# Optimization experiments

Measured on AMD Instinct MI355X. Metric: run time of the kernel, lower is better.

Reference implementation:

```python
import jax, jax.numpy as jnp
import numpy as np

C = 32
SHIFTS = (1, 2, 4)
KSIZE = 4  # trans_layer: kernel KSIZE+1, stride KSIZE, pad KSIZE//2
EPS_NORM = 1e-12
EPS_BN = 1e-5


def _make_diff_kernels(c):
    # 8 fixed 3x3 difference kernels, tiled per channel for depthwise conv.
    d1 = np.array([[[-1, 0, 0], [0, 1, 0], [0, 0, 0]],
                   [[0, -1, 0], [0, 1, 0], [0, 0, 0]],
                   [[0, 0, -1], [0, 1, 0], [0, 0, 0]],
                   [[0, 0, 0], [0, 1, -1], [0, 0, 0]]], dtype=np.float32)
    d1 = d1.reshape(4, 1, 3, 3)
    d2 = d1[:, :, ::-1, ::-1].copy()
    delta = np.concatenate([d1, d2], axis=0)          # [8,1,3,3]
    return jnp.asarray(np.tile(delta, (c, 1, 1, 1)))  # [8C,1,3,3]


DIFF_KERNELS = _make_diff_kernels(C)


def conv2d(x, w, stride=1, pad=0, dilation=1, groups=1):
    return jax.lax.conv_general_dilated(
        x, w, (stride, stride), [(pad, pad), (pad, pad)],
        rhs_dilation=(dilation, dilation),
        dimension_numbers=('NCHW', 'OIHW', 'NCHW'),
        feature_group_count=groups)


def l2norm(x, axis=-1):
    n = jnp.sqrt(jnp.sum(x * x, axis=axis, keepdims=True))
    return x / jnp.maximum(n, EPS_NORM)


def setup_inputs() -> dict:
    key = jax.random.key(0)
    ks = jax.random.split(key, 8)
    S = len(SHIFTS)
    return {
        'cen': jax.random.normal(ks[0], (2, C, 256, 256), jnp.float32),
        'trans_W': jax.random.normal(ks[1], (C, C, 5, 5), jnp.float32) * 0.05,
        'trans_b': jax.random.normal(ks[2], (C,), jnp.float32) * 0.05,
        'query_W': jax.random.normal(ks[3], (C, C, 1, 1), jnp.float32) * 0.05,
        'value_W': jax.random.normal(ks[4], (S, C, C, 1, 1), jnp.float32) * 0.05,
        'key_W': jax.random.normal(ks[5], (S, C, C, 1, 1), jnp.float32) * 0.05,
        'out_W': jax.random.normal(ks[6], (C, C, 1, 1), jnp.float32) * 0.05,
        'bn_gamma': jnp.ones((C,), jnp.float32),
        'bn_beta': jnp.zeros((C,), jnp.float32),
        'bn_mean': jnp.zeros((C,), jnp.float32),
        'bn_var': jnp.ones((C,), jnp.float32),
    }


def reference(cen, trans_W, trans_b, query_W, value_W, key_W, out_W,
              bn_gamma, bn_beta, bn_mean, bn_var):
    b, _, w, h = cen.shape
    S = len(SHIFTS)
    size = (w * h) // (KSIZE * KSIZE)

    # trans_layer: kernel KSIZE+1, stride KSIZE, pad KSIZE//2
    kv_cen = conv2d(cen, trans_W, stride=KSIZE, pad=KSIZE // 2) \
        + trans_b[None, :, None, None]

    keys, values = [], []
    for i, d in enumerate(SHIFTS):
        v = conv2d(cen, value_W[i])          # [b,C,w,h]
        k = conv2d(kv_cen, key_W[i])         # [b,C,w',h']
        # depthwise dilated difference conv -> 8 outputs per channel
        v = conv2d(v, DIFF_KERNELS, pad=d, dilation=d, groups=C)  # [b,8C,w,h]
        k = conv2d(k, DIFF_KERNELS, pad=d, dilation=d, groups=C)  # [b,8C,w',h']
        keys.append(k)
        values.append(v)

    querys = conv2d(kv_cen, query_W)  # [b,C,w',h']

    keys = jnp.stack(keys, axis=2).reshape(b, C, 8 * S, size)       # [b,C,8S,size]
    values = jnp.stack(values, axis=2).reshape(b, C, 8 * S, w * h)  # [b,C,8S,wh]

    keys = jnp.swapaxes(l2norm(keys, -1), -2, -1)        # [b,C,size,8S]
    querys = l2norm(querys.reshape(b, C, 1, size), -1)   # [b,C,1,size]

    score = jnp.matmul(querys, keys)   # [b,C,1,8S]  cosine sims
    score = l2norm(score, -1)
    out = jnp.matmul(score, values).reshape(b, C, w, h)

    # out_conv: 1x1 conv -> BN (eval mode, running stats) -> ReLU
    out = conv2d(out, out_W)
    inv = jax.lax.rsqrt(bn_var + EPS_BN)
    out = (out - bn_mean[None, :, None, None]) * (bn_gamma * inv)[None, :, None, None] \
        + bn_beta[None, :, None, None]
    return jax.nn.relu(out)
```

## Files before the change

kernel.cpp:

```cpp
#include <hip/hip_runtime.h>
#include <hip/hip_bf16.h>


#define CC 32
#define HW 256
#define KVW 64
#define VTS 100

__global__ __launch_bounds__(256, 2) void k1_trans(const float* __restrict__ cen,
                                                   const float* __restrict__ tW,
                                                   const float* __restrict__ tB,
                                                   float* __restrict__ kv) {
  __shared__ alignas(16) float part[4][4][64];
  int bid = blockIdx.x;
  int b = bid >> 9, cog = (bid >> 6) & 7, y = bid & 63;
  int tid = threadIdx.x;
  int x = tid & 63;
  int w = __builtin_amdgcn_readfirstlane(tid >> 6);
  int ci0 = w * 8;
  int co0 = cog * 4;

  float acc[4] = {0.f, 0.f, 0.f, 0.f};
  const float4 z4 = {0.f, 0.f, 0.f, 0.f};

  int roff[5];
  bool rok[5];
#pragma unroll
  for (int r = 0; r < 5; r++) {
    int row = 4 * y - 2 + r;
    rok[r] = (row >= 0);
    roff[r] = (row < 0 ? 0 : row) * HW;
  }

  for (int cc4 = 0; cc4 < 8; cc4 += 4) {
    int ci = ci0 + cc4;
    const float* pc[4];
#pragma unroll
    for (int c = 0; c < 4; c++) pc[c] = cen + (size_t)(b * CC + ci + c) * 65536 + 4 * x;
    float4 A[4][5], B[4][5];
#pragma unroll
    for (int c = 0; c < 4; c++) {
#pragma unroll
      for (int r = 0; r < 5; r++) {
        A[c][r] = (x > 0) ? *(const float4*)(pc[c] + roff[r] - 4) : z4;
        B[c][r] = *(const float4*)(pc[c] + roff[r]);
      }
    }
#pragma unroll
    for (int r = 0; r < 5; r++) {
      if (!rok[r]) continue;
#pragma unroll
      for (int c = 0; c < 4; c++) {
#pragma unroll
        for (int co = 0; co < 4; co++) {
          const float* wa = tW + ((co0 + co) * CC + ci + c) * 25 + r * 5;
          acc[co] += wa[0] * A[c][r].z + wa[1] * A[c][r].w + wa[2] * B[c][r].x +
                     wa[3] * B[c][r].y + wa[4] * B[c][r].z;
        }
      }
    }
  }

#pragma unroll
  for (int co = 0; co < 4; co++) part[w][co][x] = acc[co];
  __syncthreads();
  {
    int co = tid >> 6, xx = tid & 63;
    float s = part[0][co][xx] + part[1][co][xx] + part[2][co][xx] + part[3][co][xx];
    kv[((b * CC + co0 + co) * KVW + y) * KVW + xx] = s + tB[co0 + co];
  }
}

__device__ inline float wred64(float v) {
#pragma unroll
  for (int off = 1; off < 64; off <<= 1) v += __shfl_xor(v, off);
  return v;
}

__global__ __launch_bounds__(1024) void k23_fat(const float* __restrict__ kv,
                                                const float* __restrict__ qW,
                                                const float* __restrict__ kW,
                                                float* __restrict__ srraw,
                                                const float* __restrict__ cen,
                                                const float* __restrict__ vW,
                                                __hip_bfloat16* __restrict__ v) {
  __shared__ alignas(16) float kl[4096];
  __shared__ float wredl[16][18];
  int bid = blockIdx.x;
  int tid = threadIdx.x;
  int g = bid / 7, s = bid - g * 7;

  if (s < 3) {
    int k2id = g * 3 + s;
    int bc = k2id / 3, i = k2id - bc * 3;
    int b = bc >> 5, c = bc & 31;
    int lane = tid & 63, w = tid >> 6;
    int xx = tid & 63;
    int ybase = tid >> 6;

    float qreg[4];
#pragma unroll
    for (int r = 0; r < 4; r++) {
      int px = r * 1024 + tid;
      float q = 0.f, kk = 0.f;
#pragma unroll
      for (int ci = 0; ci < CC; ci++) {
        float val = kv[(b * CC + ci) * 4096 + px];
        q += qW[c * CC + ci] * val;
        kk += kW[(i * CC + c) * CC + ci] * val;
      }
      qreg[r] = q;
      kl[px] = kk;
    }
    __syncthreads();

    float q2 = 0.f;
#pragma unroll
    for (int r = 0; r < 4; r++) q2 += qreg[r] * qreg[r];
    q2 = wred64(q2);
    if (lane == 0) wredl[w][16] = q2;

    constexpr int DYt[8] = {-1, -1, -1, 0, 1, 1, 1, 0};
    constexpr int DXt[8] = {-1, 0, 1, 1, 1, 0, -1, -1};
    const int d = 1 << i;
#pragma unroll
    for (int n = 0; n < 8; n++) {
      const int dy = DYt[n], dx = DXt[n];
      int xn = xx + dx * d;
      bool xok = (xn >= 0 && xn < KVW);
      float dacc = 0.f, macc = 0.f;
#pragma unroll
      for (int r = 0; r < 4; r++) {
        int yy = r * 16 + ybase;
        int px = yy * KVW + xx;
        float kc = kl[px];
        int yn = yy + dy * d;
        float kn = (xok && yn >= 0 && yn < KVW) ? kl[yn * KVW + xn] : 0.f;
        float df = kc - kn;
        dacc += qreg[r] * df;
        macc += df * df;
      }
      dacc = wred64(dacc);
      macc = wred64(macc);
      if (lane == 0) {
        wredl[w][n] = dacc;
        wredl[w][8 + n] = macc;
      }
    }
    __syncthreads();

    if (tid < 8) {
      float D = 0.f, M = 0.f, Q = 0.f;
      for (int w2 = 0; w2 < 16; w2++) {
        D += wredl[w2][tid];
        M += wredl[w2][8 + tid];
        Q += wredl[w2][16];
      }
      float sr = D / (fmaxf(sqrtf(M), 1e-12f) * fmaxf(sqrtf(Q), 1e-12f));
      srraw[bc * 24 + i * 8 + tid] = sr;
    }
  } else {
    int k3id = g * 4 + (s - 3);
    int vb = k3id * 4 + (tid >> 8);
    int b = vb >> 9, blk = vb & 511;
    int lane = tid & 63;
    int cg = __builtin_amdgcn_readfirstlane((tid >> 6) & 3);
    int px = blk * 128 + lane * 2;

    float2 cr[CC];
#pragma unroll
    for (int ci = 0; ci < CC; ci++)
      cr[ci] = *(const float2*)(cen + (size_t)(b * CC + ci) * 65536 + px);

#pragma unroll
    for (int i = 0; i < 3; i++) {
#pragma unroll
      for (int cc = 0; cc < 8; cc++) {
        int c = cg * 8 + cc;
        const float* wp = vW + (i * CC + c) * CC;
        float a0 = 0.f, a1 = 0.f;
#pragma unroll
        for (int ci = 0; ci < CC; ci++) {
          a0 += wp[ci] * cr[ci].x;
          a1 += wp[ci] * cr[ci].y;
        }
        __hip_bfloat16 h0 = __float2bfloat16(a0);
        __hip_bfloat16 h1 = __float2bfloat16(a1);
        unsigned int pk = (unsigned int)(*(unsigned short*)&h0) |
                          ((unsigned int)(*(unsigned short*)&h1) << 16);
        *(unsigned int*)((unsigned short*)v + (((size_t)((i * 2 + b) * CC + c)) << 16) +
                         px) = pk;
      }
    }
  }
}

__global__ __launch_bounds__(256) void k3b_combine(const __hip_bfloat16* __restrict__ v,
                                                   const float* __restrict__ srraw,
                                                   const float* __restrict__ oW,
                                                   const float* __restrict__ gamma,
                                                   const float* __restrict__ beta,
                                                   const float* __restrict__ mean,
                                                   const float* __restrict__ var,
                                                   float* __restrict__ out) {
  __shared__ alignas(16) float vt[3 * 24 * VTS];
  __shared__ alignas(16) float sl[27][32];
  __shared__ alignas(16) float owl[32][32];
  __shared__ float bns[32], bnb[32];

  int bid = blockIdx.x;
  int b = bid >> 8, tile = bid & 255;
  int ty = tile >> 4, tx = tile & 15;
  int tid = threadIdx.x;
  int ly = tid >> 4, lx = tid & 15;

  for (int f = tid; f < 768; f += 256) {
    int j = f >> 5, c = f & 31;
    sl[j][c] = srraw[(b * CC + c) * 24 + j];
  }
  for (int f = tid; f < 1024; f += 256) owl[f >> 5][f & 31] = oW[f];
  if (tid < 32) {
    float inv = rsqrtf(var[tid] + 1e-5f);
    float sc = gamma[tid] * inv;
    bns[tid] = sc;
    bnb[tid] = beta[tid] - mean[tid] * sc;
  }
  __syncthreads();
  if (tid < 32) {
    float r2 = 0.f;
#pragma unroll
    for (int j = 0; j < 24; j++) {
      float s = sl[j][tid];
      r2 += s * s;
    }
    float dn = fmaxf(sqrtf(r2), 1e-12f);
#pragma unroll
    for (int j = 0; j < 24; j++) sl[j][tid] /= dn;
#pragma unroll
    for (int i = 0; i < 3; i++) {
      float s = 0.f;
      for (int n = 0; n < 8; n++) s += sl[i * 8 + n][tid];
      sl[24 + i][tid] = s;
    }
  }

  int ldsoff[4], pxoff[4], ibase[4];
  bool okp[4];
#pragma unroll
  for (int it = 0; it < 4; it++) {
    int p = tid + it * 256;
    bool act = (p < 864);
    int pp = act ? p : 0;
    int i = pp / 288;
    int rem = pp - i * 288;
    int r = rem / 12;
    int col = (rem - r * 12) * 2;
    int gy = ty * 16 + r - 4, gx = tx * 16 + col - 4;
    okp[it] = act && gy >= 0 && gy < HW && gx >= 0 && gx < HW;
    pxoff[it] = gy * HW + gx;
    ibase[it] = (i * 2 + b) * CC;
    ldsoff[it] = (i * 24 + r) * VTS + col * 4;
  }

  constexpr int DYt[8] = {-1, -1, -1, 0, 1, 1, 1, 0};
  constexpr int DXt[8] = {-1, 0, 1, 1, 1, 0, -1, -1};

  float acc[32];
#pragma unroll
  for (int co = 0; co < 32; co++) acc[co] = 0.f;

  unsigned int pf[4][4];
  const unsigned short* vs = (const unsigned short*)v;

#pragma unroll
  for (int it = 0; it < 4; it++)
#pragma unroll
    for (int cp = 0; cp < 4; cp++)
      pf[it][cp] = okp[it]
                       ? *(const unsigned int*)(vs + (((size_t)(ibase[it] + cp)) << 16) +
                                                pxoff[it])
                       : 0u;

  for (int cg = 0; cg < 8; cg++) {
    __syncthreads();
#pragma unroll
    for (int it = 0; it < 4; it++) {
      if (it == 3 && tid >= 96) continue;
      float4 lo, hi;
      lo.x = __uint_as_float(pf[it][0] << 16);
      lo.y = __uint_as_float(pf[it][1] << 16);
      lo.z = __uint_as_float(pf[it][2] << 16);
      lo.w = __uint_as_float(pf[it][3] << 16);
      hi.x = __uint_as_float(pf[it][0] & 0xffff0000u);
      hi.y = __uint_as_float(pf[it][1] & 0xffff0000u);
      hi.z = __uint_as_float(pf[it][2] & 0xffff0000u);
      hi.w = __uint_as_float(pf[it][3] & 0xffff0000u);
      *(float4*)&vt[ldsoff[it]] = lo;
      *(float4*)&vt[ldsoff[it] + 4] = hi;
    }
    if (cg < 7) {
      int cb = (cg + 1) * 4;
#pragma unroll
      for (int it = 0; it < 4; it++)
#pragma unroll
        for (int cp = 0; cp < 4; cp++)
          pf[it][cp] = okp[it] ? *(const unsigned int*)(vs +
                                                        (((size_t)(ibase[it] + cb + cp))
                                                         << 16) +
                                                        pxoff[it])
                               : 0u;
    }
    __syncthreads();

    float4 pre = {0.f, 0.f, 0.f, 0.f};
#pragma unroll
    for (int i = 0; i < 3; i++) {
      const int d = 1 << i;
      float4 S4 = *(const float4*)&sl[24 + i][cg * 4];
      float4 ctr = *(const float4*)&vt[(i * 24 + (ly + 4)) * VTS + (lx + 4) * 4];
      pre.x += S4.x * ctr.x;
      pre.y += S4.y * ctr.y;
      pre.z += S4.z * ctr.z;
      pre.w += S4.w * ctr.w;
#pragma unroll
      for (int n = 0; n < 8; n++) {
        float4 sj = *(const float4*)&sl[i * 8 + n][cg * 4];
        float4 nb = *(const float4*)&vt[(i * 24 + (ly + 4 + DYt[n] * d)) * VTS +
                                        (lx + 4 + DXt[n] * d) * 4];
        pre.x -= sj.x * nb.x;
        pre.y -= sj.y * nb.y;
        pre.z -= sj.z * nb.z;
        pre.w -= sj.w * nb.w;
      }
    }
#pragma unroll
    for (int co = 0; co < 32; co++) {
      float4 ow = *(const float4*)&owl[co][cg * 4];
      acc[co] += ow.x * pre.x + ow.y * pre.y + ow.z * pre.z + ow.w * pre.w;
    }
  }

  int gy = ty * 16 + ly, gx = tx * 16 + lx;
#pragma unroll
  for (int co = 0; co < 32; co++) {
    float val = acc[co] * bns[co] + bnb[co];
    out[((size_t)(b * CC + co) << 16) + gy * HW + gx] = fmaxf(val, 0.f);
  }
}

extern "C" void kernel_launch(void* const* d_in, const int* in_sizes, int n_in,
                              void* d_out, int out_size, void* d_ws, size_t ws_size,
                              hipStream_t stream) {
  const float* cen = (const float*)d_in[0];
  const float* trans_W = (const float*)d_in[1];
  const float* trans_b = (const float*)d_in[2];
  const float* query_W = (const float*)d_in[3];
  const float* value_W = (const float*)d_in[4];
  const float* key_W = (const float*)d_in[5];
  const float* out_W = (const float*)d_in[6];
  const float* bn_gamma = (const float*)d_in[7];
  const float* bn_beta = (const float*)d_in[8];
  const float* bn_mean = (const float*)d_in[9];
  const float* bn_var = (const float*)d_in[10];
  float* out = (float*)d_out;

  float* kv = (float*)d_out;
  float* srraw = (float*)d_ws;
  __hip_bfloat16* v = (__hip_bfloat16*)((char*)d_ws + 532480);

  k1_trans<<<1024, 256, 0, stream>>>(cen, trans_W, trans_b, kv);
  k23_fat<<<448, 1024, 0, stream>>>(kv, query_W, key_W, srraw, cen, value_W, v);
  k3b_combine<<<512, 256, 0, stream>>>(v, srraw, out_W, bn_gamma, bn_beta, bn_mean,
                                       bn_var, out);
}
```

Measured before the change: 161.1 us.

## Store value tensor channel-last bf16 and read stencil neighbors directly from global

The value projection now writes bf16 values in a pixel-major, channel-contiguous layout (32 channels per pixel) using 16-byte vector stores. The combine kernel drops the LDS halo tile, its double-buffered prefetch and its per-channel-group syncs. Each thread instead loads each neighbor's 32 channels as four uint4 reads straight from global/L2. It also folds the negation into the normalized scores, reads out_W from global instead of LDS, and swizzles the block order. This trades LDS staging and barriers for more redundant global/cache traffic across the 27 stencil taps.

```diff
diff --git a/kernel.cpp b/kernel.cpp
--- a/kernel.cpp
+++ b/kernel.cpp
@@ -5,7 +5,6 @@
 #define CC 32
 #define HW 256
 #define KVW 64
-#define VTS 100
 
 __global__ __launch_bounds__(256, 2) void k1_trans(const float* __restrict__ cen,
                                                    const float* __restrict__ tW,
@@ -172,25 +171,38 @@
     for (int ci = 0; ci < CC; ci++)
       cr[ci] = *(const float2*)(cen + (size_t)(b * CC + ci) * 65536 + px);
 
+    unsigned short* vo = (unsigned short*)v;
 #pragma unroll
     for (int i = 0; i < 3; i++) {
-#pragma unroll
-      for (int cc = 0; cc < 8; cc++) {
-        int c = cg * 8 + cc;
-        const float* wp = vW + (i * CC + c) * CC;
-        float a0 = 0.f, a1 = 0.f;
+      unsigned int d0[4], d1[4];
+#pragma unroll
+      for (int cp = 0; cp < 4; cp++) {
+        int c0 = cg * 8 + cp * 2;
+        const float* wpA = vW + (i * CC + c0) * CC;
+        const float* wpB = wpA + CC;
+        float a0A = 0.f, a1A = 0.f, a0B = 0.f, a1B = 0.f;
 #pragma unroll
         for (int ci = 0; ci < CC; ci++) {
-          a0 += wp[ci] * cr[ci].x;
-          a1 += wp[ci] * cr[ci].y;
+          a0A += wpA[ci] * cr[ci].x;
+          a1A += wpA[ci] * cr[ci].y;
+          a0B += wpB[ci] * cr[ci].x;
+          a1B += wpB[ci] * cr[ci].y;
         }
-        __hip_bfloat16 h0 = __float2bfloat16(a0);
-        __hip_bfloat16 h1 = __float2bfloat16(a1);
-        unsigned int pk = (unsigned int)(*(unsigned short*)&h0) |
-                          ((unsigned int)(*(unsigned short*)&h1) << 16);
-        *(unsigned int*)((unsigned short*)v + (((size_t)((i * 2 + b) * CC + c)) << 16) +
-                         px) = pk;
-      }
+        __hip_bfloat16 hA0 = __float2bfloat16(a0A);
+        __hip_bfloat16 hB0 = __float2bfloat16(a0B);
+        __hip_bfloat16 hA1 = __float2bfloat16(a1A);
+        __hip_bfloat16 hB1 = __float2bfloat16(a1B);
+        d0[cp] = (unsigned int)(*(unsigned short*)&hA0) |
+                 ((unsigned int)(*(unsigned short*)&hB0) << 16);
+        d1[cp] = (unsigned int)(*(unsigned short*)&hA1) |
+                 ((unsigned int)(*(unsigned short*)&hB1) << 16);
+      }
+      size_t base = ((size_t)((i * 2 + b) * 65536 + px)) * 32 + cg * 8;
+      uint4 q0, q1;
+      q0.x = d0[0]; q0.y = d0[1]; q0.z = d0[2]; q0.w = d0[3];
+      q1.x = d1[0]; q1.y = d1[1]; q1.z = d1[2]; q1.w = d1[3];
+      *(uint4*)(vo + base) = q0;
+      *(uint4*)(vo + base + 32) = q1;
     }
   }
 }
@@ -203,22 +215,21 @@
                                                    const float* __restrict__ mean,
                                                    const float* __restrict__ var,
                                                    float* __restrict__ out) {
-  __shared__ alignas(16) float vt[3 * 24 * VTS];
   __shared__ alignas(16) float sl[27][32];
-  __shared__ alignas(16) float owl[32][32];
   __shared__ float bns[32], bnb[32];
 
-  int bid = blockIdx.x;
+  int bid0 = blockIdx.x;
+  int bid = (bid0 & 7) * 64 + (bid0 >> 3);
   int b = bid >> 8, tile = bid & 255;
   int ty = tile >> 4, tx = tile & 15;
   int tid = threadIdx.x;
   int ly = tid >> 4, lx = tid & 15;
+  int y = ty * 16 + ly, x = tx * 16 + lx;
 
   for (int f = tid; f < 768; f += 256) {
     int j = f >> 5, c = f & 31;
     sl[j][c] = srraw[(b * CC + c) * 24 + j];
   }
-  for (int f = tid; f < 1024; f += 256) owl[f >> 5][f & 31] = oW[f];
   if (tid < 32) {
     float inv = rsqrtf(var[tid] + 1e-5f);
     float sc = gamma[tid] * inv;
@@ -235,116 +246,72 @@
     }
     float dn = fmaxf(sqrtf(r2), 1e-12f);
 #pragma unroll
-    for (int j = 0; j < 24; j++) sl[j][tid] /= dn;
-#pragma unroll
     for (int i = 0; i < 3; i++) {
-      float s = 0.f;
-      for (int n = 0; n < 8; n++) s += sl[i * 8 + n][tid];
-      sl[24 + i][tid] = s;
-    }
-  }
-
-  int ldsoff[4], pxoff[4], ibase[4];
-  bool okp[4];
-#pragma unroll
-  for (int it = 0; it < 4; it++) {
-    int p = tid + it * 256;
-    bool act = (p < 864);
-    int pp = act ? p : 0;
-    int i = pp / 288;
-    int rem = pp - i * 288;
-    int r = rem / 12;
-    int col = (rem - r * 12) * 2;
-    int gy = ty * 16 + r - 4, gx = tx * 16 + col - 4;
-    okp[it] = act && gy >= 0 && gy < HW && gx >= 0 && gx < HW;
-    pxoff[it] = gy * HW + gx;
-    ibase[it] = (i * 2 + b) * CC;
-    ldsoff[it] = (i * 24 + r) * VTS + col * 4;
-  }
+      float ssum = 0.f;
+#pragma unroll
+      for (int n = 0; n < 8; n++) {
+        float sn = sl[i * 8 + n][tid] / dn;
+        sl[i * 8 + n][tid] = -sn;
+        ssum += sn;
+      }
+      sl[24 + i][tid] = ssum;
+    }
+  }
+  __syncthreads();
 
   constexpr int DYt[8] = {-1, -1, -1, 0, 1, 1, 1, 0};
   constexpr int DXt[8] = {-1, 0, 1, 1, 1, 0, -1, -1};
 
-  float acc[32];
-#pragma unroll
-  for (int co = 0; co < 32; co++) acc[co] = 0.f;
-
-  unsigned int pf[4][4];
   const unsigned short* vs = (const unsigned short*)v;
-
-#pragma unroll
-  for (int it = 0; it < 4; it++)
-#pragma unroll
-    for (int cp = 0; cp < 4; cp++)
-      pf[it][cp] = okp[it]
-                       ? *(const unsigned int*)(vs + (((size_t)(ibase[it] + cp)) << 16) +
-                                                pxoff[it])
-                       : 0u;
-
-  for (int cg = 0; cg < 8; cg++) {
-    __syncthreads();
-#pragma unroll
-    for (int it = 0; it < 4; it++) {
-      if (it == 3 && tid >= 96) continue;
-      float4 lo, hi;
-      lo.x = __uint_as_float(pf[it][0] << 16);
-      lo.y = __uint_as_float(pf[it][1] << 16);
-      lo.z = __uint_as_float(pf[it][2] << 16);
-      lo.w = __uint_as_float(pf[it][3] << 16);
-      hi.x = __uint_as_float(pf[it][0] & 0xffff0000u);
-      hi.y = __uint_as_float(pf[it][1] & 0xffff0000u);
-      hi.z = __uint_as_float(pf[it][2] & 0xffff0000u);
-      hi.w = __uint_as_float(pf[it][3] & 0xffff0000u);
-      *(float4*)&vt[ldsoff[it]] = lo;
-      *(float4*)&vt[ldsoff[it] + 4] = hi;
-    }
-    if (cg < 7) {
-      int cb = (cg + 1) * 4;
-#pragma unroll
-      for (int it = 0; it < 4; it++)
-#pragma unroll
-        for (int cp = 0; cp < 4; cp++)
-          pf[it][cp] = okp[it] ? *(const unsigned int*)(vs +
-                                                        (((size_t)(ibase[it] + cb + cp))
-                                                         << 16) +
-                                                        pxoff[it])
-                               : 0u;
-    }
-    __syncthreads();
-
-    float4 pre = {0.f, 0.f, 0.f, 0.f};
-#pragma unroll
-    for (int i = 0; i < 3; i++) {
-      const int d = 1 << i;
-      float4 S4 = *(const float4*)&sl[24 + i][cg * 4];
-      float4 ctr = *(const float4*)&vt[(i * 24 + (ly + 4)) * VTS + (lx + 4) * 4];
-      pre.x += S4.x * ctr.x;
-      pre.y += S4.y * ctr.y;
-      pre.z += S4.z * ctr.z;
-      pre.w += S4.w * ctr.w;
-#pragma unroll
-      for (int n = 0; n < 8; n++) {
-        float4 sj = *(const float4*)&sl[i * 8 + n][cg * 4];
-        float4 nb = *(const float4*)&vt[(i * 24 + (ly + 4 + DYt[n] * d)) * VTS +
-                                        (lx + 4 + DXt[n] * d) * 4];
-        pre.x -= sj.x * nb.x;
-        pre.y -= sj.y * nb.y;
-        pre.z -= sj.z * nb.z;
-        pre.w -= sj.w * nb.w;
-      }
-    }
-#pragma unroll
-    for (int co = 0; co < 32; co++) {
-      float4 ow = *(const float4*)&owl[co][cg * 4];
-      acc[co] += ow.x * pre.x + ow.y * pre.y + ow.z * pre.z + ow.w * pre.w;
-    }
-  }
-
-  int gy = ty * 16 + ly, gx = tx * 16 + lx;
-#pragma unroll
-  for (int co = 0; co < 32; co++) {
-    float val = acc[co] * bns[co] + bnb[co];
-    out[((size_t)(b * CC + co) << 16) + gy * HW + gx] = fmaxf(val, 0.f);
+  float4 pre[8];
+#pragma unroll
+  for (int j = 0; j < 8; j++) pre[j] = {0.f, 0.f, 0.f, 0.f};
+
+#pragma unroll
+  for (int i = 0; i < 3; i++) {
+    const int d = 1 << i;
+#pragma unroll
+    for (int t = 0; t < 9; t++) {
+      const int dy = (t == 0) ? 0 : DYt[t - 1];
+      const int dx = (t == 0) ? 0 : DXt[t - 1];
+      const int srow = (t == 0) ? 24 + i : i * 8 + (t - 1);
+      int py = y + dy * d, px = x + dx * d;
+      bool ok = (py >= 0 && py < HW && px >= 0 && px < HW);
+      uint4 qa = {0u, 0u, 0u, 0u}, qb = qa, qc = qa, qd = qa;
+      if (ok) {
+        const unsigned short* p =
+            vs + ((size_t)((i * 2 + b) * 65536 + py * HW + px)) * 32;
+        qa = *(const uint4*)p;
+        qb = *(const uint4*)(p + 8);
+        qc = *(const uint4*)(p + 16);
+        qd = *(const uint4*)(p + 24);
+      }
+      unsigned int dw[16] = {qa.x, qa.y, qa.z, qa.w, qb.x, qb.y, qb.z, qb.w,
+                             qc.x, qc.y, qc.z, qc.w, qd.x, qd.y, qd.z, qd.w};
+#pragma unroll
+      for (int j = 0; j < 8; j++) {
+        float4 w4 = *(const float4*)&sl[srow][j * 4];
+        unsigned int u0 = dw[2 * j], u1 = dw[2 * j + 1];
+        pre[j].x += w4.x * __uint_as_float(u0 << 16);
+        pre[j].y += w4.y * __uint_as_float(u0 & 0xffff0000u);
+        pre[j].z += w4.z * __uint_as_float(u1 << 16);
+        pre[j].w += w4.w * __uint_as_float(u1 & 0xffff0000u);
+      }
+    }
+  }
+
+  int opx = y * HW + x;
+#pragma unroll
+  for (int co = 0; co < CC; co++) {
+    const float* owr = oW + co * CC;
+    float s = 0.f;
+#pragma unroll
+    for (int j = 0; j < 8; j++) {
+      float4 w = *(const float4*)(owr + j * 4);
+      s += w.x * pre[j].x + w.y * pre[j].y + w.z * pre[j].z + w.w * pre[j].w;
+    }
+    float val = s * bns[co] + bnb[co];
+    out[((size_t)(b * CC + co) << 16) + opx] = fmaxf(val, 0.f);
   }
 }
 
```

Result: slower. 338.9 us (+110.4%).
